# Performance work log

Hardware: AMD Instinct MI355X
Metric: run time of the kernel (lower is better)

Reference implementation:

```python
import jax, jax.numpy as jnp
import numpy as np

N_ENT = 50000
N_EDGE = 500000
D = 256          # ent_hidden_size
H1, C1 = 8, 64   # conv1: heads=8, out=64, concat -> 512
NEG_SLOPE = 0.2
LN_EPS = 1e-5


def setup_inputs() -> dict:
    key = jax.random.key(0)
    ks = jax.random.split(key, 12)
    s = 0.05  # small init scale for numerical sanity
    return {
        "edge_index": jax.random.randint(ks[0], (2, N_EDGE), 0, N_ENT),
        "x": jax.random.normal(ks[1], (N_ENT, D), dtype=jnp.float32),
        "ln_w": jnp.ones((D,), jnp.float32),
        "ln_b": jnp.zeros((D,), jnp.float32),
        "W1": jax.random.normal(ks[2], (D, H1 * C1), dtype=jnp.float32) * s,
        "att_src1": jax.random.normal(ks[3], (H1, C1), dtype=jnp.float32) * s,
        "att_dst1": jax.random.normal(ks[4], (H1, C1), dtype=jnp.float32) * s,
        "b1": jnp.zeros((H1 * C1,), jnp.float32),
        "W2": jax.random.normal(ks[5], (H1 * C1, D), dtype=jnp.float32) * s,
        "att_src2": jax.random.normal(ks[6], (1, D), dtype=jnp.float32) * s,
        "att_dst2": jax.random.normal(ks[7], (1, D), dtype=jnp.float32) * s,
        "b2": jnp.zeros((D,), jnp.float32),
    }


def _gat_conv(x, edge_index, W, att_src, att_dst, bias, heads, out_ch, concat):
    """PyG GATConv (shared src/dst lin, add_self_loops=True, eval-mode dropout)."""
    n = x.shape[0]
    loops = jnp.arange(n)
    src = jnp.concatenate([edge_index[0], loops])  # [E+N]
    dst = jnp.concatenate([edge_index[1], loops])

    h = (x @ W).reshape(n, heads, out_ch)                 # [N,H,C]
    a_src = jnp.sum(h * att_src[None], axis=-1)           # [N,H]
    a_dst = jnp.sum(h * att_dst[None], axis=-1)           # [N,H]

    e = jax.nn.leaky_relu(a_src[src] + a_dst[dst], NEG_SLOPE)  # [E+N,H]
    # per-destination segment softmax (every dst has a self-loop -> no empties)
    m = jax.lax.stop_gradient(jax.ops.segment_max(e, dst, num_segments=n))
    p = jnp.exp(e - m[dst])
    denom = jax.ops.segment_sum(p, dst, num_segments=n)
    alpha = p / denom[dst]                                # [E+N,H]

    out = jax.ops.segment_sum(h[src] * alpha[..., None], dst, num_segments=n)  # [N,H,C]
    out = out.reshape(n, heads * out_ch) if concat else out.mean(axis=1)
    return out + bias


def reference(edge_index, x, ln_w, ln_b, W1, att_src1, att_dst1, b1,
              W2, att_src2, att_dst2, b2):
    # LayerNorm(ent_hidden), eps=1e-5; dropouts are eval-mode no-ops
    mu = jnp.mean(x, axis=-1, keepdims=True)
    var = jnp.var(x, axis=-1, keepdims=True)
    h = (x - mu) / jnp.sqrt(var + LN_EPS) * ln_w + ln_b
    h = jax.nn.elu(_gat_conv(h, edge_index, W1, att_src1, att_dst1, b1, H1, C1, True))
    return _gat_conv(h, edge_index, W2, att_src2, att_dst2, b2, 1, D, False)
```

## Files before the change

kernel.cpp:

```cpp
#include <hip/hip_runtime.h>
#include <hip/hip_bf16.h>
#include <cstdint>

#define N_ENT  50000
#define N_EDGE 500000
#define D_IN   256
#define CAP    64

typedef __attribute__((ext_vector_type(8))) short bfrag;
typedef __attribute__((ext_vector_type(4))) float f4acc;
typedef __attribute__((ext_vector_type(4))) float f32x4;
typedef __attribute__((ext_vector_type(8))) short s16x8;

__device__ __forceinline__ float lrelu(float x) { return x > 0.f ? x : 0.2f * x; }
__device__ __forceinline__ float eluf(float x)  { return x > 0.f ? x : (expf(x) - 1.f); }
__device__ __forceinline__ short to_bf16(float f) {
    __hip_bfloat16 b = __float2bfloat16(f);
    return *(short*)&b;
}
__device__ __forceinline__ float2 bf2_to_f32(unsigned int u) {
    float2 r;
    r.x = __uint_as_float(u << 16);
    r.y = __uint_as_float(u & 0xffff0000u);
    return r;
}

__global__ __launch_bounds__(256) void prep_kernel(const float* __restrict__ x,
        const float* __restrict__ lnw, const float* __restrict__ lnb,
        short* __restrict__ y, const int* __restrict__ ei,
        int* __restrict__ cursor2, int* __restrict__ csr_src,
        const float* __restrict__ W1, short* __restrict__ W1T,
        const float* __restrict__ W2, short* __restrict__ W2T,
        const float* __restrict__ att_s1, const float* __restrict__ att_d1,
        const float* __restrict__ att_s2, const float* __restrict__ att_d2,
        short* __restrict__ wAttT, float* __restrict__ v2s, float* __restrict__ v2d)
{
    int blk = blockIdx.x;
    if (blk < 1954) {
        int e = blk * 256 + threadIdx.x;
        if (e < N_EDGE) {
            int d = ei[N_EDGE + e];
            int pos = atomicAdd(&cursor2[d], 1);
            if (pos < CAP) csr_src[(d << 6) + pos] = ei[e];
        }
    } else if (blk < 14454) {
        int n = (blk - 1954) * 4 + (threadIdx.x >> 6);
        int lane = threadIdx.x & 63;
        const f32x4 v = __builtin_nontemporal_load((const f32x4*)(x + (size_t)n * D_IN + lane * 4));
        float s  = v.x + v.y + v.z + v.w;
        float sq = v.x*v.x + v.y*v.y + v.z*v.z + v.w*v.w;
        #pragma unroll
        for (int off = 1; off < 64; off <<= 1) {
            s  += __shfl_xor(s, off);
            sq += __shfl_xor(sq, off);
        }
        float mean = s * (1.f / 256.f);
        float var  = sq * (1.f / 256.f) - mean * mean;
        float rstd = rsqrtf(var + 1e-5f);
        float4 wv = *(const float4*)(lnw + lane * 4);
        float4 bv = *(const float4*)(lnb + lane * 4);
        short4 o;
        o.x = to_bf16((v.x - mean) * rstd * wv.x + bv.x);
        o.y = to_bf16((v.y - mean) * rstd * wv.y + bv.y);
        o.z = to_bf16((v.z - mean) * rstd * wv.z + bv.z);
        o.w = to_bf16((v.w - mean) * rstd * wv.w + bv.w);
        *(short4*)(y + (size_t)n * D_IN + lane * 4) = o;
    } else if (blk < 14966) {
        int i = (blk - 14454) * 256 + threadIdx.x;
        int r = i >> 9, c = i & 511;
        W1T[c * 256 + r] = to_bf16(W1[i]);
    } else if (blk < 15478) {
        int i = (blk - 14966) * 256 + threadIdx.x;
        int r = i >> 8, c = i & 255;
        W2T[c * 512 + r] = to_bf16(W2[i]);
    } else if (blk == 15478) {
        int k = threadIdx.x;
        const float* wrow = W1 + (size_t)k * 512;
        #pragma unroll
        for (int h = 0; h < 8; ++h) {
            float ws = 0.f, wd = 0.f;
            #pragma unroll
            for (int c4 = 0; c4 < 16; ++c4) {
                float4 wv = *(const float4*)(wrow + h * 64 + c4 * 4);
                float4 as = *(const float4*)(att_s1 + h * 64 + c4 * 4);
                float4 ad = *(const float4*)(att_d1 + h * 64 + c4 * 4);
                ws += wv.x*as.x + wv.y*as.y + wv.z*as.z + wv.w*as.w;
                wd += wv.x*ad.x + wv.y*ad.y + wv.z*ad.z + wv.w*ad.w;
            }
            wAttT[h * 256 + k]       = to_bf16(ws);
            wAttT[(8 + h) * 256 + k] = to_bf16(wd);
        }
    } else {
        int t = threadIdx.x;
        #pragma unroll
        for (int kk = 0; kk < 2; ++kk) {
            int k = t + kk * 256;
            const float* wrow = W2 + (size_t)k * 256;
            float vs = 0.f, vd = 0.f;
            for (int c4 = 0; c4 < 64; ++c4) {
                float4 wv = *(const float4*)(wrow + c4 * 4);
                float4 as = *(const float4*)(att_s2 + c4 * 4);
                float4 ad = *(const float4*)(att_d2 + c4 * 4);
                vs += wv.x*as.x + wv.y*as.y + wv.z*as.z + wv.w*as.w;
                vd += wv.x*ad.x + wv.y*ad.y + wv.z*ad.z + wv.w*ad.w;
            }
            v2s[k] = vs;
            v2d[k] = vd;
        }
    }
}

template<int NN, int KK, bool TAIL>
__global__ __launch_bounds__(256) void gemm_mfma(const short* __restrict__ A,
        const short* __restrict__ BT, short* __restrict__ C, int M, int nGemm,
        const short* __restrict__ wAttT, float* __restrict__ a_s, float* __restrict__ a_d)
{
    constexpr int GX = NN / 128;
    constexpr int NK = KK / 32;
    __shared__ __align__(16) short As[2][128 * 32];
    __shared__ __align__(16) short Bs[2][128 * 32];

    if (TAIL && (int)blockIdx.x >= nGemm) {
        int bb = (int)blockIdx.x - nGemm;
        int w = threadIdx.x >> 6, l = threadIdx.x & 63;
        int ln16 = l & 15, q = l >> 4;
        int r0 = bb * 64 + w * 16;
        if (r0 >= M) return;
        bfrag bfv[8];
        #pragma unroll
        for (int kk = 0; kk < 8; ++kk)
            bfv[kk] = *(const bfrag*)(wAttT + ln16 * 256 + kk * 32 + q * 8);
        f4acc acc = (f4acc){0.f, 0.f, 0.f, 0.f};
        #pragma unroll
        for (int kk = 0; kk < 8; ++kk) {
            bfrag af = *(const bfrag*)(A + (size_t)(r0 + ln16) * 256 + kk * 32 + q * 8);
            acc = __builtin_amdgcn_mfma_f32_16x16x32_bf16(af, bfv[kk], acc, 0, 0, 0);
        }
        #pragma unroll
        for (int p = 0; p < 4; ++p) {
            int r = r0 + q * 4 + p;
            if (ln16 < 8) a_s[(size_t)r * 8 + ln16]     = acc[p];
            else          a_d[(size_t)r * 8 + ln16 - 8] = acc[p];
        }
        return;
    }

    const int tid  = threadIdx.x;
    const int w    = tid >> 6;
    const int l    = tid & 63;
    const int wm   = w >> 1, wn = w & 1;
    const int m0   = ((int)blockIdx.x / GX) * 128;
    const int n0   = ((int)blockIdx.x % GX) * 128;
    const int quad = l >> 4;
    const int ln16 = l & 15;
    const int rl   = l >> 2;
    const int cs   = l & 3;

    f4acc acc[4][4];
    #pragma unroll
    for (int i = 0; i < 4; ++i)
        #pragma unroll
        for (int j = 0; j < 4; ++j)
            acc[i][j] = (f4acc){0.f, 0.f, 0.f, 0.f};

    auto stage = [&](int k0, int b) {
        #pragma unroll
        for (int tt = 0; tt < 2; ++tt) {
            int t   = w * 2 + tt;
            int row = t * 16 + rl;
            int ca  = cs ^ ((row >> 1) & 3);
            const short* ga = A + (size_t)(m0 + row) * KK + k0 + ca * 8;
            __builtin_amdgcn_global_load_lds(
                (const __attribute__((address_space(1))) unsigned int*)ga,
                (__attribute__((address_space(3))) unsigned int*)&As[b][t * 512], 16, 0, 0);
            const short* gb = BT + (size_t)(n0 + row) * KK + k0 + ca * 8;
            __builtin_amdgcn_global_load_lds(
                (const __attribute__((address_space(1))) unsigned int*)gb,
                (__attribute__((address_space(3))) unsigned int*)&Bs[b][t * 512], 16, 0, 0);
        }
    };

    stage(0, 0);
    int cur = 0;
    for (int ks = 0; ks < NK; ++ks) {
        __syncthreads();
        if (ks + 1 < NK) stage((ks + 1) * 32, cur ^ 1);
        bfrag af[4], bf[4];
        #pragma unroll
        for (int i = 0; i < 4; ++i) {
            int r = wm * 64 + i * 16 + ln16;
            af[i] = *(const bfrag*)&As[cur][r * 32 + (quad ^ ((r >> 1) & 3)) * 8];
            int rn = wn * 64 + i * 16 + ln16;
            bf[i] = *(const bfrag*)&Bs[cur][rn * 32 + (quad ^ ((rn >> 1) & 3)) * 8];
        }
        #pragma unroll
        for (int i = 0; i < 4; ++i)
            #pragma unroll
            for (int j = 0; j < 4; ++j)
                acc[i][j] = __builtin_amdgcn_mfma_f32_16x16x32_bf16(af[i], bf[j], acc[i][j], 0, 0, 0);
        cur ^= 1;
    }

    #pragma unroll
    for (int i = 0; i < 4; ++i) {
        #pragma unroll
        for (int p = 0; p < 4; ++p) {
            int gr = m0 + wm * 64 + i * 16 + quad * 4 + p;
            if (gr < M) {
                #pragma unroll
                for (int j = 0; j < 4; ++j) {
                    int gc = n0 + wn * 64 + j * 16 + ln16;
                    C[(size_t)gr * NN + gc] = to_bf16(acc[i][j][p]);
                }
            }
        }
    }
}

__global__ __launch_bounds__(256) void aggr1_kernel(const int* __restrict__ csr_src,
        const int* __restrict__ cnt,
        const short* __restrict__ feat, const float* __restrict__ a_s,
        const float* __restrict__ a_d, const float* __restrict__ bias,
        short* __restrict__ out,
        const float* __restrict__ v2s, const float* __restrict__ v2d,
        float* __restrict__ a_s2, float* __restrict__ a_d2)
{
    int d = blockIdx.x * 4 + (threadIdx.x >> 6);
    if (d >= N_ENT) return;
    int lane = threadIdx.x & 63;
    int f0 = lane * 8;
    int h = lane >> 3;
    int rs = d << 6;
    int n = min(cnt[d], CAP);
    int myidx = (lane < n) ? csr_src[rs + lane] : d;
    float adh = a_d[d * 8 + h];

    float den = 0.f;
    float acc[8] = {0.f, 0.f, 0.f, 0.f, 0.f, 0.f, 0.f, 0.f};
    {
        float p = __expf(lrelu(a_s[d * 8 + h] + adh));
        den += p;
        uint4 rv = *(const uint4*)(feat + (size_t)d * 512 + f0);
        float2 t0 = bf2_to_f32(rv.x), t1 = bf2_to_f32(rv.y);
        float2 t2 = bf2_to_f32(rv.z), t3 = bf2_to_f32(rv.w);
        acc[0] += p * t0.x; acc[1] += p * t0.y; acc[2] += p * t1.x; acc[3] += p * t1.y;
        acc[4] += p * t2.x; acc[5] += p * t2.y; acc[6] += p * t3.x; acc[7] += p * t3.y;
    }
    for (int i = 0; i < n; i += 8) {
        int   sv[8];
        float ev[8];
        uint4 rv[8];
        #pragma unroll
        for (int u = 0; u < 8; ++u) sv[u] = __shfl(myidx, i + u);
        #pragma unroll
        for (int u = 0; u < 8; ++u) ev[u] = a_s[sv[u] * 8 + h];
        #pragma unroll
        for (int u = 0; u < 8; ++u) rv[u] = *(const uint4*)(feat + (size_t)sv[u] * 512 + f0);
        #pragma unroll
        for (int u = 0; u < 8; ++u) {
            float p = (i + u < n) ? __expf(lrelu(ev[u] + adh)) : 0.f;
            den += p;
            float2 t0 = bf2_to_f32(rv[u].x), t1 = bf2_to_f32(rv[u].y);
            float2 t2 = bf2_to_f32(rv[u].z), t3 = bf2_to_f32(rv[u].w);
            acc[0] += p * t0.x; acc[1] += p * t0.y; acc[2] += p * t1.x; acc[3] += p * t1.y;
            acc[4] += p * t2.x; acc[5] += p * t2.y; acc[6] += p * t3.x; acc[7] += p * t3.y;
        }
    }
    float inv = 1.f / den;
    float4 b0 = *(const float4*)(bias + f0);
    float4 b1 = *(const float4*)(bias + f0 + 4);
    float hv[8];
    hv[0] = eluf(acc[0] * inv + b0.x); hv[1] = eluf(acc[1] * inv + b0.y);
    hv[2] = eluf(acc[2] * inv + b0.z); hv[3] = eluf(acc[3] * inv + b0.w);
    hv[4] = eluf(acc[4] * inv + b1.x); hv[5] = eluf(acc[5] * inv + b1.y);
    hv[6] = eluf(acc[6] * inv + b1.z); hv[7] = eluf(acc[7] * inv + b1.w);

    float4 s0 = *(const float4*)(v2s + f0), s1 = *(const float4*)(v2s + f0 + 4);
    float4 d0 = *(const float4*)(v2d + f0), d1 = *(const float4*)(v2d + f0 + 4);
    float ds = hv[0]*s0.x + hv[1]*s0.y + hv[2]*s0.z + hv[3]*s0.w
             + hv[4]*s1.x + hv[5]*s1.y + hv[6]*s1.z + hv[7]*s1.w;
    float dd = hv[0]*d0.x + hv[1]*d0.y + hv[2]*d0.z + hv[3]*d0.w
             + hv[4]*d1.x + hv[5]*d1.y + hv[6]*d1.z + hv[7]*d1.w;
    #pragma unroll
    for (int off = 1; off < 64; off <<= 1) {
        ds += __shfl_xor(ds, off);
        dd += __shfl_xor(dd, off);
    }
    if (lane == 0) { a_s2[d] = ds; a_d2[d] = dd; }

    s16x8 o;
    o[0] = to_bf16(hv[0]); o[1] = to_bf16(hv[1]);
    o[2] = to_bf16(hv[2]); o[3] = to_bf16(hv[3]);
    o[4] = to_bf16(hv[4]); o[5] = to_bf16(hv[5]);
    o[6] = to_bf16(hv[6]); o[7] = to_bf16(hv[7]);
    __builtin_nontemporal_store(o, (s16x8*)(out + (size_t)d * 512 + f0));
}

__global__ __launch_bounds__(256) void aggr2_kernel(const int* __restrict__ csr_src,
        const int* __restrict__ cnt,
        const short* __restrict__ feat, const float* __restrict__ a_s,
        const float* __restrict__ a_d, const float* __restrict__ bias,
        float* __restrict__ out)
{
    int d = blockIdx.x * 4 + (threadIdx.x >> 6);
    if (d >= N_ENT) return;
    int lane = threadIdx.x & 63;
    int half = lane >> 5;
    int li   = lane & 31;
    int f0   = li * 8;
    int rs = d << 6;
    int n = min(cnt[d], CAP);
    int myidx = (lane < n) ? csr_src[rs + lane] : d;
    float adh = a_d[d];

    float den = 0.f;
    float acc[8] = {0.f, 0.f, 0.f, 0.f, 0.f, 0.f, 0.f, 0.f};
    {
        float p = (half == 0) ? __expf(lrelu(a_s[d] + adh)) : 0.f;
        uint4 rv = *(const uint4*)(feat + (size_t)d * 256 + f0);
        den += p;
        float2 t0 = bf2_to_f32(rv.x), t1 = bf2_to_f32(rv.y);
        float2 t2 = bf2_to_f32(rv.z), t3 = bf2_to_f32(rv.w);
        acc[0] += p * t0.x; acc[1] += p * t0.y; acc[2] += p * t1.x; acc[3] += p * t1.y;
        acc[4] += p * t2.x; acc[5] += p * t2.y; acc[6] += p * t3.x; acc[7] += p * t3.y;
    }
    for (int i = 0; i < n; i += 8) {
        int   sv[4];
        float av[4];
        uint4 rv[4];
        #pragma unroll
        for (int u = 0; u < 4; ++u) sv[u] = __shfl(myidx, i + 2 * u + half);
        #pragma unroll
        for (int u = 0; u < 4; ++u) av[u] = a_s[sv[u]];
        #pragma unroll
        for (int u = 0; u < 4; ++u) rv[u] = *(const uint4*)(feat + (size_t)sv[u] * 256 + f0);
        #pragma unroll
        for (int u = 0; u < 4; ++u) {
            float p = (i + 2 * u + half < n) ? __expf(lrelu(av[u] + adh)) : 0.f;
            den += p;
            float2 t0 = bf2_to_f32(rv[u].x), t1 = bf2_to_f32(rv[u].y);
            float2 t2 = bf2_to_f32(rv[u].z), t3 = bf2_to_f32(rv[u].w);
            acc[0] += p * t0.x; acc[1] += p * t0.y; acc[2] += p * t1.x; acc[3] += p * t1.y;
            acc[4] += p * t2.x; acc[5] += p * t2.y; acc[6] += p * t3.x; acc[7] += p * t3.y;
        }
    }
    den += __shfl_xor(den, 32);
    #pragma unroll
    for (int k = 0; k < 8; ++k) acc[k] += __shfl_xor(acc[k], 32);

    float inv = 1.f / den;
    if (half == 0) {
        float4 b0 = *(const float4*)(bias + f0);
        float4 b1 = *(const float4*)(bias + f0 + 4);
        f32x4 o0, o1;
        o0.x = acc[0] * inv + b0.x; o0.y = acc[1] * inv + b0.y;
        o0.z = acc[2] * inv + b0.z; o0.w = acc[3] * inv + b0.w;
        o1.x = acc[4] * inv + b1.x; o1.y = acc[5] * inv + b1.y;
        o1.z = acc[6] * inv + b1.z; o1.w = acc[7] * inv + b1.w;
        __builtin_nontemporal_store(o0, (f32x4*)(out + (size_t)d * 256 + f0));
        __builtin_nontemporal_store(o1, (f32x4*)(out + (size_t)d * 256 + f0 + 4));
    }
}

extern "C" void kernel_launch(void* const* d_in, const int* in_sizes, int n_in,
                              void* d_out, int out_size, void* d_ws, size_t ws_size,
                              hipStream_t stream)
{
    const int*   ei     = (const int*)  d_in[0];
    const float* x      = (const float*)d_in[1];
    const float* ln_w   = (const float*)d_in[2];
    const float* ln_b   = (const float*)d_in[3];
    const float* W1     = (const float*)d_in[4];
    const float* att_s1 = (const float*)d_in[5];
    const float* att_d1 = (const float*)d_in[6];
    const float* b1     = (const float*)d_in[7];
    const float* W2     = (const float*)d_in[8];
    const float* att_s2 = (const float*)d_in[9];
    const float* att_d2 = (const float*)d_in[10];
    const float* b2     = (const float*)d_in[11];
    float* out = (float*)d_out;

    short* h0b = (short*)d_ws;
    short* h1b = h0b + 12800000;
    short* h2b = h1b + 25600000;
    short* h3b = h2b + 25600000;
    short* W1T = h3b + 12800000;
    short* W2T = W1T + 131072;
    short* wAttT = W2T + 131072;
    float* a_s1 = (float*)(wAttT + 4096);
    float* a_d1 = a_s1 + 400000;
    float* a_s2 = a_d1 + 400000;
    float* a_d2 = a_s2 + 50000;
    float* v2s  = a_d2 + 50000;
    float* v2d  = v2s + 512;
    int* cursor2   = (int*)(v2d + 512);
    int* csr_src   = cursor2 + 50000;

    hipMemsetAsync(cursor2, 0, 50000 * 4, stream);

    prep_kernel<<<15480, 256, 0, stream>>>(x, ln_w, ln_b, h0b, ei, cursor2, csr_src,
                                           W1, W1T, W2, W2T,
                                           att_s1, att_d1, att_s2, att_d2, wAttT, v2s, v2d);

    constexpr int NG1 = 391 * 4;
    constexpr int ND1 = 782;
    gemm_mfma<512, 256, true><<<NG1 + ND1, 256, 0, stream>>>(
        h0b, W1T, h1b, N_ENT, NG1, wAttT, a_s1, a_d1);
    aggr1_kernel<<<12500, 256, 0, stream>>>(csr_src, cursor2, h1b, a_s1, a_d1, b1, h2b,
                                            v2s, v2d, a_s2, a_d2);

    constexpr int NG2 = 391 * 2;
    gemm_mfma<256, 512, false><<<NG2, 256, 0, stream>>>(
        h2b, W2T, h3b, N_ENT, NG2, nullptr, nullptr, nullptr);
    aggr2_kernel<<<12500, 256, 0, stream>>>(csr_src, cursor2, h3b, a_s2, a_d2, b2, out);
}
```

Baseline: 365.6 us.

## Split GAT aggregation across heads/column chunks with edge-parallel lanes and atomic attention dots

```diff
diff --git a/kernel.cpp b/kernel.cpp
--- a/kernel.cpp
+++ b/kernel.cpp
@@ -225,75 +225,75 @@
         const float* __restrict__ v2s, const float* __restrict__ v2d,
         float* __restrict__ a_s2, float* __restrict__ a_d2)
 {
-    int d = blockIdx.x * 4 + (threadIdx.x >> 6);
-    if (d >= N_ENT) return;
+    int blk = blockIdx.x;
+    int h = blk & 7;
+    int d = (blk >> 3) * 4 + (threadIdx.x >> 6);
     int lane = threadIdx.x & 63;
-    int f0 = lane * 8;
-    int h = lane >> 3;
+    int g  = lane >> 3;
+    int cl = lane & 7;
     int rs = d << 6;
     int n = min(cnt[d], CAP);
-    int myidx = (lane < n) ? csr_src[rs + lane] : d;
+    int m = n + 1;
     float adh = a_d[d * 8 + h];
 
     float den = 0.f;
     float acc[8] = {0.f, 0.f, 0.f, 0.f, 0.f, 0.f, 0.f, 0.f};
-    {
-        float p = __expf(lrelu(a_s[d * 8 + h] + adh));
+    for (int i = 0; i < m; i += 8) {
+        int e = i + g;
+        bool val = e < m;
+        int src = d;
+        if (val && e > 0) src = csr_src[rs + e - 1];
+        float as = a_s[src * 8 + h];
+        uint4 rv = *(const uint4*)(feat + (size_t)src * 512 + h * 64 + cl * 8);
+        float p = val ? __expf(lrelu(as + adh)) : 0.f;
         den += p;
-        uint4 rv = *(const uint4*)(feat + (size_t)d * 512 + f0);
         float2 t0 = bf2_to_f32(rv.x), t1 = bf2_to_f32(rv.y);
         float2 t2 = bf2_to_f32(rv.z), t3 = bf2_to_f32(rv.w);
         acc[0] += p * t0.x; acc[1] += p * t0.y; acc[2] += p * t1.x; acc[3] += p * t1.y;
         acc[4] += p * t2.x; acc[5] += p * t2.y; acc[6] += p * t3.x; acc[7] += p * t3.y;
     }
-    for (int i = 0; i < n; i += 8) {
-        int   sv[8];
-        float ev[8];
-        uint4 rv[8];
-        #pragma unroll
-        for (int u = 0; u < 8; ++u) sv[u] = __shfl(myidx, i + u);
-        #pragma unroll
-        for (int u = 0; u < 8; ++u) ev[u] = a_s[sv[u] * 8 + h];
-        #pragma unroll
-        for (int u = 0; u < 8; ++u) rv[u] = *(const uint4*)(feat + (size_t)sv[u] * 512 + f0);
-        #pragma unroll
-        for (int u = 0; u < 8; ++u) {
-            float p = (i + u < n) ? __expf(lrelu(ev[u] + adh)) : 0.f;
-            den += p;
-            float2 t0 = bf2_to_f32(rv[u].x), t1 = bf2_to_f32(rv[u].y);
-            float2 t2 = bf2_to_f32(rv[u].z), t3 = bf2_to_f32(rv[u].w);
-            acc[0] += p * t0.x; acc[1] += p * t0.y; acc[2] += p * t1.x; acc[3] += p * t1.y;
-            acc[4] += p * t2.x; acc[5] += p * t2.y; acc[6] += p * t3.x; acc[7] += p * t3.y;
-        }
+    #pragma unroll
+    for (int off = 8; off < 64; off <<= 1) {
+        den += __shfl_xor(den, off);
+        #pragma unroll
+        for (int k = 0; k < 8; ++k) acc[k] += __shfl_xor(acc[k], off);
     }
     float inv = 1.f / den;
-    float4 b0 = *(const float4*)(bias + f0);
-    float4 b1 = *(const float4*)(bias + f0 + 4);
+    int c0 = h * 64 + cl * 8;
+    float4 b0 = *(const float4*)(bias + c0);
+    float4 b1 = *(const float4*)(bias + c0 + 4);
     float hv[8];
     hv[0] = eluf(acc[0] * inv + b0.x); hv[1] = eluf(acc[1] * inv + b0.y);
     hv[2] = eluf(acc[2] * inv + b0.z); hv[3] = eluf(acc[3] * inv + b0.w);
     hv[4] = eluf(acc[4] * inv + b1.x); hv[5] = eluf(acc[5] * inv + b1.y);
     hv[6] = eluf(acc[6] * inv + b1.z); hv[7] = eluf(acc[7] * inv + b1.w);
 
-    float4 s0 = *(const float4*)(v2s + f0), s1 = *(const float4*)(v2s + f0 + 4);
-    float4 d0 = *(const float4*)(v2d + f0), d1 = *(const float4*)(v2d + f0 + 4);
+    float4 s0 = *(const float4*)(v2s + c0), s1 = *(const float4*)(v2s + c0 + 4);
+    float4 d0 = *(const float4*)(v2d + c0), d1 = *(const float4*)(v2d + c0 + 4);
     float ds = hv[0]*s0.x + hv[1]*s0.y + hv[2]*s0.z + hv[3]*s0.w
              + hv[4]*s1.x + hv[5]*s1.y + hv[6]*s1.z + hv[7]*s1.w;
     float dd = hv[0]*d0.x + hv[1]*d0.y + hv[2]*d0.z + hv[3]*d0.w
              + hv[4]*d1.x + hv[5]*d1.y + hv[6]*d1.z + hv[7]*d1.w;
-    #pragma unroll
-    for (int off = 1; off < 64; off <<= 1) {
-        ds += __shfl_xor(ds, off);
-        dd += __shfl_xor(dd, off);
-    }
-    if (lane == 0) { a_s2[d] = ds; a_d2[d] = dd; }
-
-    s16x8 o;
-    o[0] = to_bf16(hv[0]); o[1] = to_bf16(hv[1]);
-    o[2] = to_bf16(hv[2]); o[3] = to_bf16(hv[3]);
-    o[4] = to_bf16(hv[4]); o[5] = to_bf16(hv[5]);
-    o[6] = to_bf16(hv[6]); o[7] = to_bf16(hv[7]);
-    __builtin_nontemporal_store(o, (s16x8*)(out + (size_t)d * 512 + f0));
+    if (g == 0) {
+        #pragma unroll
+        for (int off = 1; off < 8; off <<= 1) {
+            ds += __shfl_xor(ds, off);
+            dd += __shfl_xor(dd, off);
+        }
+        if (cl == 0) {
+            unsafeAtomicAdd(&a_s2[d], ds);
+            unsafeAtomicAdd(&a_d2[d], dd);
+        }
+    }
+
+    if (g == 0) {
+        s16x8 o;
+        o[0] = to_bf16(hv[0]); o[1] = to_bf16(hv[1]);
+        o[2] = to_bf16(hv[2]); o[3] = to_bf16(hv[3]);
+        o[4] = to_bf16(hv[4]); o[5] = to_bf16(hv[5]);
+        o[6] = to_bf16(hv[6]); o[7] = to_bf16(hv[7]);
+        __builtin_nontemporal_store(o, (s16x8*)(out + (size_t)d * 512 + c0));
+    }
 }
 
 __global__ __launch_bounds__(256) void aggr2_kernel(const int* __restrict__ csr_src,
@@ -302,63 +302,51 @@
         const float* __restrict__ a_d, const float* __restrict__ bias,
         float* __restrict__ out)
 {
-    int d = blockIdx.x * 4 + (threadIdx.x >> 6);
-    if (d >= N_ENT) return;
+    int blk = blockIdx.x;
+    int c = blk & 7;
+    int d = (blk >> 3) * 4 + (threadIdx.x >> 6);
     int lane = threadIdx.x & 63;
-    int half = lane >> 5;
-    int li   = lane & 31;
-    int f0   = li * 8;
+    int g  = lane >> 2;
+    int cl = lane & 3;
     int rs = d << 6;
     int n = min(cnt[d], CAP);
-    int myidx = (lane < n) ? csr_src[rs + lane] : d;
+    int m = n + 1;
     float adh = a_d[d];
 
     float den = 0.f;
     float acc[8] = {0.f, 0.f, 0.f, 0.f, 0.f, 0.f, 0.f, 0.f};
-    {
-        float p = (half == 0) ? __expf(lrelu(a_s[d] + adh)) : 0.f;
-        uint4 rv = *(const uint4*)(feat + (size_t)d * 256 + f0);
+    for (int i = 0; i < m; i += 16) {
+        int e = i + g;
+        bool val = e < m;
+        int src = d;
+        if (val && e > 0) src = csr_src[rs + e - 1];
+        float as = a_s[src];
+        uint4 rv = *(const uint4*)(feat + (size_t)src * 256 + c * 32 + cl * 8);
+        float p = val ? __expf(lrelu(as + adh)) : 0.f;
         den += p;
         float2 t0 = bf2_to_f32(rv.x), t1 = bf2_to_f32(rv.y);
         float2 t2 = bf2_to_f32(rv.z), t3 = bf2_to_f32(rv.w);
         acc[0] += p * t0.x; acc[1] += p * t0.y; acc[2] += p * t1.x; acc[3] += p * t1.y;
         acc[4] += p * t2.x; acc[5] += p * t2.y; acc[6] += p * t3.x; acc[7] += p * t3.y;
     }
-    for (int i = 0; i < n; i += 8) {
-        int   sv[4];
-        float av[4];
-        uint4 rv[4];
-        #pragma unroll
-        for (int u = 0; u < 4; ++u) sv[u] = __shfl(myidx, i + 2 * u + half);
-        #pragma unroll
-        for (int u = 0; u < 4; ++u) av[u] = a_s[sv[u]];
-        #pragma unroll
-        for (int u = 0; u < 4; ++u) rv[u] = *(const uint4*)(feat + (size_t)sv[u] * 256 + f0);
-        #pragma unroll
-        for (int u = 0; u < 4; ++u) {
-            float p = (i + 2 * u + half < n) ? __expf(lrelu(av[u] + adh)) : 0.f;
-            den += p;
-            float2 t0 = bf2_to_f32(rv[u].x), t1 = bf2_to_f32(rv[u].y);
-            float2 t2 = bf2_to_f32(rv[u].z), t3 = bf2_to_f32(rv[u].w);
-            acc[0] += p * t0.x; acc[1] += p * t0.y; acc[2] += p * t1.x; acc[3] += p * t1.y;
-            acc[4] += p * t2.x; acc[5] += p * t2.y; acc[6] += p * t3.x; acc[7] += p * t3.y;
-        }
-    }
-    den += __shfl_xor(den, 32);
     #pragma unroll
-    for (int k = 0; k < 8; ++k) acc[k] += __shfl_xor(acc[k], 32);
-
+    for (int off = 4; off < 64; off <<= 1) {
+        den += __shfl_xor(den, off);
+        #pragma unroll
+        for (int k = 0; k < 8; ++k) acc[k] += __shfl_xor(acc[k], off);
+    }
     float inv = 1.f / den;
-    if (half == 0) {
-        float4 b0 = *(const float4*)(bias + f0);
-        float4 b1 = *(const float4*)(bias + f0 + 4);
+    if (g == 0) {
+        int c0 = c * 32 + cl * 8;
+        float4 b0 = *(const float4*)(bias + c0);
+        float4 b1 = *(const float4*)(bias + c0 + 4);
         f32x4 o0, o1;
         o0.x = acc[0] * inv + b0.x; o0.y = acc[1] * inv + b0.y;
         o0.z = acc[2] * inv + b0.z; o0.w = acc[3] * inv + b0.w;
         o1.x = acc[4] * inv + b1.x; o1.y = acc[5] * inv + b1.y;
         o1.z = acc[6] * inv + b1.z; o1.w = acc[7] * inv + b1.w;
-        __builtin_nontemporal_store(o0, (f32x4*)(out + (size_t)d * 256 + f0));
-        __builtin_nontemporal_store(o1, (f32x4*)(out + (size_t)d * 256 + f0 + 4));
+        __builtin_nontemporal_store(o0, (f32x4*)(out + (size_t)d * 256 + c0));
+        __builtin_nontemporal_store(o1, (f32x4*)(out + (size_t)d * 256 + c0 + 4));
     }
 }
 
@@ -389,14 +377,14 @@
     short* wAttT = W2T + 131072;
     float* a_s1 = (float*)(wAttT + 4096);
     float* a_d1 = a_s1 + 400000;
-    float* a_s2 = a_d1 + 400000;
+    float* v2s  = a_d1 + 400000;
+    float* v2d  = v2s + 512;
+    float* a_s2 = v2d + 512;
     float* a_d2 = a_s2 + 50000;
-    float* v2s  = a_d2 + 50000;
-    float* v2d  = v2s + 512;
-    int* cursor2   = (int*)(v2d + 512);
+    int* cursor2   = (int*)(a_d2 + 50000);
     int* csr_src   = cursor2 + 50000;
 
-    hipMemsetAsync(cursor2, 0, 50000 * 4, stream);
+    hipMemsetAsync(a_s2, 0, 150000 * 4, stream);
 
     prep_kernel<<<15480, 256, 0, stream>>>(x, ln_w, ln_b, h0b, ei, cursor2, csr_src,
                                            W1, W1T, W2, W2T,
@@ -406,11 +394,11 @@
     constexpr int ND1 = 782;
     gemm_mfma<512, 256, true><<<NG1 + ND1, 256, 0, stream>>>(
         h0b, W1T, h1b, N_ENT, NG1, wAttT, a_s1, a_d1);
-    aggr1_kernel<<<12500, 256, 0, stream>>>(csr_src, cursor2, h1b, a_s1, a_d1, b1, h2b,
-                                            v2s, v2d, a_s2, a_d2);
+    aggr1_kernel<<<12500 * 8, 256, 0, stream>>>(csr_src, cursor2, h1b, a_s1, a_d1, b1, h2b,
+                                                v2s, v2d, a_s2, a_d2);
 
     constexpr int NG2 = 391 * 2;
     gemm_mfma<256, 512, false><<<NG2, 256, 0, stream>>>(
         h2b, W2T, h3b, N_ENT, NG2, nullptr, nullptr, nullptr);
-    aggr2_kernel<<<12500, 256, 0, stream>>>(csr_src, cursor2, h3b, a_s2, a_d2, b2, out);
-}
+    aggr2_kernel<<<12500 * 8, 256, 0, stream>>>(csr_src, cursor2, h3b, a_s2, a_d2, b2, out);
+}
```

Result: slower. 607.9 us (+66.3%).

## Store layer-2 features in column-chunked layout and split aggr2 by channel slice

Applied to the files above, without the earlier changes.

```diff
diff --git a/kernel.cpp b/kernel.cpp
--- a/kernel.cpp
+++ b/kernel.cpp
@@ -110,7 +110,7 @@
     }
 }
 
-template<int NN, int KK, bool TAIL>
+template<int NN, int KK, bool TAIL, bool SWZC>
 __global__ __launch_bounds__(256) void gemm_mfma(const short* __restrict__ A,
         const short* __restrict__ BT, short* __restrict__ C, int M, int nGemm,
         const short* __restrict__ wAttT, float* __restrict__ a_s, float* __restrict__ a_d)
@@ -210,7 +210,11 @@
                 #pragma unroll
                 for (int j = 0; j < 4; ++j) {
                     int gc = n0 + wn * 64 + j * 16 + ln16;
-                    C[(size_t)gr * NN + gc] = to_bf16(acc[i][j][p]);
+                    if constexpr (SWZC)
+                        C[(size_t)(gc >> 5) * ((size_t)N_ENT * 32) + (size_t)gr * 32 + (gc & 31)]
+                            = to_bf16(acc[i][j][p]);
+                    else
+                        C[(size_t)gr * NN + gc] = to_bf16(acc[i][j][p]);
                 }
             }
         }
@@ -232,7 +236,6 @@
     int h = lane >> 3;
     int rs = d << 6;
     int n = min(cnt[d], CAP);
-    int myidx = (lane < n) ? csr_src[rs + lane] : d;
     float adh = a_d[d * 8 + h];
 
     float den = 0.f;
@@ -246,25 +249,36 @@
         acc[0] += p * t0.x; acc[1] += p * t0.y; acc[2] += p * t1.x; acc[3] += p * t1.y;
         acc[4] += p * t2.x; acc[5] += p * t2.y; acc[6] += p * t3.x; acc[7] += p * t3.y;
     }
-    for (int i = 0; i < n; i += 8) {
-        int   sv[8];
-        float ev[8];
-        uint4 rv[8];
-        #pragma unroll
-        for (int u = 0; u < 8; ++u) sv[u] = __shfl(myidx, i + u);
-        #pragma unroll
-        for (int u = 0; u < 8; ++u) ev[u] = a_s[sv[u] * 8 + h];
-        #pragma unroll
-        for (int u = 0; u < 8; ++u) rv[u] = *(const uint4*)(feat + (size_t)sv[u] * 512 + f0);
-        #pragma unroll
-        for (int u = 0; u < 8; ++u) {
-            float p = (i + u < n) ? __expf(lrelu(ev[u] + adh)) : 0.f;
+    int i = 0;
+    for (; i + 4 <= n; i += 4) {
+        int   sv[4];
+        float ev[4];
+        uint4 rv[4];
+        #pragma unroll
+        for (int u = 0; u < 4; ++u) sv[u] = csr_src[rs + i + u];
+        #pragma unroll
+        for (int u = 0; u < 4; ++u) ev[u] = a_s[sv[u] * 8 + h];
+        #pragma unroll
+        for (int u = 0; u < 4; ++u) rv[u] = *(const uint4*)(feat + (size_t)sv[u] * 512 + f0);
+        #pragma unroll
+        for (int u = 0; u < 4; ++u) {
+            float p = __expf(lrelu(ev[u] + adh));
             den += p;
             float2 t0 = bf2_to_f32(rv[u].x), t1 = bf2_to_f32(rv[u].y);
             float2 t2 = bf2_to_f32(rv[u].z), t3 = bf2_to_f32(rv[u].w);
             acc[0] += p * t0.x; acc[1] += p * t0.y; acc[2] += p * t1.x; acc[3] += p * t1.y;
             acc[4] += p * t2.x; acc[5] += p * t2.y; acc[6] += p * t3.x; acc[7] += p * t3.y;
         }
+    }
+    for (; i < n; ++i) {
+        int s = csr_src[rs + i];
+        float p = __expf(lrelu(a_s[s * 8 + h] + adh));
+        den += p;
+        uint4 rv = *(const uint4*)(feat + (size_t)s * 512 + f0);
+        float2 t0 = bf2_to_f32(rv.x), t1 = bf2_to_f32(rv.y);
+        float2 t2 = bf2_to_f32(rv.z), t3 = bf2_to_f32(rv.w);
+        acc[0] += p * t0.x; acc[1] += p * t0.y; acc[2] += p * t1.x; acc[3] += p * t1.y;
+        acc[4] += p * t2.x; acc[5] += p * t2.y; acc[6] += p * t3.x; acc[7] += p * t3.y;
     }
     float inv = 1.f / den;
     float4 b0 = *(const float4*)(bias + f0);
@@ -302,64 +316,61 @@
         const float* __restrict__ a_d, const float* __restrict__ bias,
         float* __restrict__ out)
 {
-    int d = blockIdx.x * 4 + (threadIdx.x >> 6);
+    int c    = blockIdx.x & 7;
+    int wid  = threadIdx.x >> 6;
+    int lane = threadIdx.x & 63;
+    int g    = lane >> 2;
+    int cl   = lane & 3;
+    int d    = ((int)blockIdx.x >> 3) * 64 + wid * 16 + g;
     if (d >= N_ENT) return;
-    int lane = threadIdx.x & 63;
-    int half = lane >> 5;
-    int li   = lane & 31;
-    int f0   = li * 8;
     int rs = d << 6;
     int n = min(cnt[d], CAP);
-    int myidx = (lane < n) ? csr_src[rs + lane] : d;
     float adh = a_d[d];
-
-    float den = 0.f;
-    float acc[8] = {0.f, 0.f, 0.f, 0.f, 0.f, 0.f, 0.f, 0.f};
+    const short* fb = feat + (size_t)c * ((size_t)N_ENT * 32) + cl * 8;
+
+    float den;
+    float acc[8];
     {
-        float p = (half == 0) ? __expf(lrelu(a_s[d] + adh)) : 0.f;
-        uint4 rv = *(const uint4*)(feat + (size_t)d * 256 + f0);
-        den += p;
+        float p = __expf(lrelu(a_s[d] + adh));
+        den = p;
+        uint4 rv = *(const uint4*)(fb + (size_t)d * 32);
         float2 t0 = bf2_to_f32(rv.x), t1 = bf2_to_f32(rv.y);
         float2 t2 = bf2_to_f32(rv.z), t3 = bf2_to_f32(rv.w);
-        acc[0] += p * t0.x; acc[1] += p * t0.y; acc[2] += p * t1.x; acc[3] += p * t1.y;
-        acc[4] += p * t2.x; acc[5] += p * t2.y; acc[6] += p * t3.x; acc[7] += p * t3.y;
-    }
-    for (int i = 0; i < n; i += 8) {
+        acc[0] = p * t0.x; acc[1] = p * t0.y; acc[2] = p * t1.x; acc[3] = p * t1.y;
+        acc[4] = p * t2.x; acc[5] = p * t2.y; acc[6] = p * t3.x; acc[7] = p * t3.y;
+    }
+    for (int i = 0; i < n; i += 4) {
+        int idxl = (i + cl < n) ? csr_src[rs + i + cl] : d;
         int   sv[4];
         float av[4];
         uint4 rv[4];
         #pragma unroll
-        for (int u = 0; u < 4; ++u) sv[u] = __shfl(myidx, i + 2 * u + half);
-        #pragma unroll
-        for (int u = 0; u < 4; ++u) av[u] = a_s[sv[u]];
-        #pragma unroll
-        for (int u = 0; u < 4; ++u) rv[u] = *(const uint4*)(feat + (size_t)sv[u] * 256 + f0);
-        #pragma unroll
-        for (int u = 0; u < 4; ++u) {
-            float p = (i + 2 * u + half < n) ? __expf(lrelu(av[u] + adh)) : 0.f;
+        for (int e = 0; e < 4; ++e) sv[e] = __shfl(idxl, (g << 2) | e);
+        #pragma unroll
+        for (int e = 0; e < 4; ++e) av[e] = a_s[sv[e]];
+        #pragma unroll
+        for (int e = 0; e < 4; ++e) rv[e] = *(const uint4*)(fb + (size_t)sv[e] * 32);
+        #pragma unroll
+        for (int e = 0; e < 4; ++e) {
+            float p = (i + e < n) ? __expf(lrelu(av[e] + adh)) : 0.f;
             den += p;
-            float2 t0 = bf2_to_f32(rv[u].x), t1 = bf2_to_f32(rv[u].y);
-            float2 t2 = bf2_to_f32(rv[u].z), t3 = bf2_to_f32(rv[u].w);
+            float2 t0 = bf2_to_f32(rv[e].x), t1 = bf2_to_f32(rv[e].y);
+            float2 t2 = bf2_to_f32(rv[e].z), t3 = bf2_to_f32(rv[e].w);
             acc[0] += p * t0.x; acc[1] += p * t0.y; acc[2] += p * t1.x; acc[3] += p * t1.y;
             acc[4] += p * t2.x; acc[5] += p * t2.y; acc[6] += p * t3.x; acc[7] += p * t3.y;
         }
     }
-    den += __shfl_xor(den, 32);
-    #pragma unroll
-    for (int k = 0; k < 8; ++k) acc[k] += __shfl_xor(acc[k], 32);
-
     float inv = 1.f / den;
-    if (half == 0) {
-        float4 b0 = *(const float4*)(bias + f0);
-        float4 b1 = *(const float4*)(bias + f0 + 4);
-        f32x4 o0, o1;
-        o0.x = acc[0] * inv + b0.x; o0.y = acc[1] * inv + b0.y;
-        o0.z = acc[2] * inv + b0.z; o0.w = acc[3] * inv + b0.w;
-        o1.x = acc[4] * inv + b1.x; o1.y = acc[5] * inv + b1.y;
-        o1.z = acc[6] * inv + b1.z; o1.w = acc[7] * inv + b1.w;
-        __builtin_nontemporal_store(o0, (f32x4*)(out + (size_t)d * 256 + f0));
-        __builtin_nontemporal_store(o1, (f32x4*)(out + (size_t)d * 256 + f0 + 4));
-    }
+    int c0 = c * 32 + cl * 8;
+    float4 b0 = *(const float4*)(bias + c0);
+    float4 b1 = *(const float4*)(bias + c0 + 4);
+    f32x4 o0, o1;
+    o0.x = acc[0] * inv + b0.x; o0.y = acc[1] * inv + b0.y;
+    o0.z = acc[2] * inv + b0.z; o0.w = acc[3] * inv + b0.w;
+    o1.x = acc[4] * inv + b1.x; o1.y = acc[5] * inv + b1.y;
+    o1.z = acc[6] * inv + b1.z; o1.w = acc[7] * inv + b1.w;
+    __builtin_nontemporal_store(o0, (f32x4*)(out + (size_t)d * 256 + c0));
+    __builtin_nontemporal_store(o1, (f32x4*)(out + (size_t)d * 256 + c0 + 4));
 }
 
 extern "C" void kernel_launch(void* const* d_in, const int* in_sizes, int n_in,
@@ -404,13 +415,13 @@
 
     constexpr int NG1 = 391 * 4;
     constexpr int ND1 = 782;
-    gemm_mfma<512, 256, true><<<NG1 + ND1, 256, 0, stream>>>(
+    gemm_mfma<512, 256, true, false><<<NG1 + ND1, 256, 0, stream>>>(
         h0b, W1T, h1b, N_ENT, NG1, wAttT, a_s1, a_d1);
     aggr1_kernel<<<12500, 256, 0, stream>>>(csr_src, cursor2, h1b, a_s1, a_d1, b1, h2b,
                                             v2s, v2d, a_s2, a_d2);
 
     constexpr int NG2 = 391 * 2;
-    gemm_mfma<256, 512, false><<<NG2, 256, 0, stream>>>(
+    gemm_mfma<256, 512, false, true><<<NG2, 256, 0, stream>>>(
         h2b, W2T, h3b, N_ENT, NG2, nullptr, nullptr, nullptr);
-    aggr2_kernel<<<12500, 256, 0, stream>>>(csr_src, cursor2, h3b, a_s2, a_d2, b2, out);
-}
+    aggr2_kernel<<<782 * 8, 256, 0, stream>>>(csr_src, cursor2, h3b, a_s2, a_d2, b2, out);
+}
```

Measured after the change: 379.1 us. +3.7%, slower.
